# Kernel optimization log

Measured on AMD Instinct MI355X. Metric: run time of the kernel, lower is better.

## Reference

```python
import jax, jax.numpy as jnp
import numpy as np

B, N, DEG = 64, 512, 16        # graphs, nodes per graph, avg degree
C, HID = 10, 128               # input feat dim (== num_classes quirk), hidden
E = B * N * DEG                # total edges (fixed; pooling masks edges)


def _gcn(x, W, b, src, dst, emask, n):
    # PyG GCNConv: add self-loops, symmetric norm D^-1/2 (A+I) D^-1/2 (XW) + b
    h = x @ W
    deg = jax.ops.segment_sum(emask, dst, num_segments=n) + 1.0  # +1 self-loop
    dinv = jax.lax.rsqrt(deg)
    norm = dinv[src] * dinv[dst] * emask
    agg = jax.ops.segment_sum(h[src] * norm[:, None], dst, num_segments=n)
    return agg + h * (dinv * dinv)[:, None] + b  # self-loop term + bias


def _sag_pool(x, src, dst, emask, Wp, bp, n_per):
    # SAGPooling: score = tanh(GCN(x)); per-graph top-k (ratio=0.5); x' = x[perm]*score
    n = x.shape[0]
    score = jnp.tanh(_gcn(x, Wp, bp, src, dst, emask, n)[:, 0])
    k = n_per // 2
    vals, idx = jax.lax.top_k(score.reshape(B, n_per), k)  # [B,k]
    perm = (idx + (jnp.arange(B) * n_per)[:, None]).reshape(-1)
    xk = x[perm] * vals.reshape(-1)[:, None]
    # relabel edges; drop edges touching removed nodes via mask (fixed E)
    mapping = jnp.full((n,), -1, jnp.int32).at[perm].set(
        jnp.arange(B * k, dtype=jnp.int32))
    ns, nd = mapping[src], mapping[dst]
    nmask = emask * ((ns >= 0) & (nd >= 0)).astype(emask.dtype)
    return xk, jnp.maximum(ns, 0), jnp.maximum(nd, 0), nmask, k


def _readout(x, k):
    # global max pool || global mean pool (all kept nodes are real, no padding)
    xg = x.reshape(B, k, -1)
    return jnp.concatenate([xg.max(axis=1), xg.mean(axis=1)], axis=1)


def setup_inputs() -> dict:
    key = jax.random.key(0)
    ks = jax.random.split(key, 16)
    x = jax.random.normal(ks[0], (B * N, C), jnp.float32)
    off = jnp.repeat(jnp.arange(B, dtype=jnp.int32) * N, N * DEG)
    src = jax.random.randint(ks[1], (E,), 0, N, jnp.int32) + off
    dst = jax.random.randint(ks[2], (E,), 0, N, jnp.int32) + off
    p = lambda k, s: jax.random.normal(k, s, jnp.float32) * 0.05
    return {
        "x": x, "src": src, "dst": dst,
        "W1": p(ks[3], (C, HID)), "b1": jnp.zeros((HID,), jnp.float32),
        "W2": p(ks[4], (HID, HID)), "b2": jnp.zeros((HID,), jnp.float32),
        "W3": p(ks[5], (HID, HID)), "b3": jnp.zeros((HID,), jnp.float32),
        "Wp": p(ks[6], (HID, 1)), "bp": jnp.zeros((1,), jnp.float32),
        "L1W": p(ks[7], (2 * HID, HID)), "L1b": jnp.zeros((HID,), jnp.float32),
        "L2W": p(ks[8], (HID, HID // 2)), "L2b": jnp.zeros((HID // 2,), jnp.float32),
    }


def reference(x, src, dst, W1, b1, W2, b2, W3, b3, Wp, bp, L1W, L1b, L2W, L2b):
    emask = jnp.ones((E,), jnp.float32)
    h = jax.nn.relu(_gcn(x, W1, b1, src, dst, emask, B * N))
    h, src, dst, emask, k = _sag_pool(h, src, dst, emask, Wp, bp, N)
    x1 = _readout(h, k)
    h = jax.nn.relu(_gcn(h, W2, b2, src, dst, emask, B * k))
    h, src, dst, emask, k = _sag_pool(h, src, dst, emask, Wp, bp, k)
    x2 = _readout(h, k)
    h = jax.nn.relu(_gcn(h, W3, b3, src, dst, emask, B * k))
    h, src, dst, emask, k = _sag_pool(h, src, dst, emask, Wp, bp, k)
    x3 = _readout(h, k)
    z = x1 + x2 + x3
    z = jax.nn.relu(z @ L1W + L1b)
    # dropout inactive in eval mode
    z = jax.nn.relu(z @ L2W + L2b)
    return jax.nn.log_softmax(z, axis=1)
```

## Files before the change

### kernel.cpp

```cpp
#include <hip/hip_runtime.h>
#include <math.h>

#define BGR 64
#define N0 512
#define E_TOT (BGR*N0*16)
#define EPG 8192
#define EIT 16
#define HID 128


__global__ __launch_bounds__(512) void k_topo0(
    const int* __restrict__ s0, const int* __restrict__ d0,
    int2* __restrict__ edges, int* __restrict__ cnt, int* __restrict__ rowptr,
    float* __restrict__ dinv, int2* __restrict__ csr, float* __restrict__ z){
  __shared__ int   deg[512];
  __shared__ int   sb[512];
  __shared__ int   cur[512];
  __shared__ float dl[512];
  int g = (blockIdx.x & 7)*8 + (blockIdx.x >> 3);
  int t = threadIdx.x;
  int gbase = g*N0, ebase = g*EPG;
  deg[t] = 0;
  if (t < 256) z[g*256 + t] = 0.f;
  __syncthreads();
  int2 ebuf[EIT];
  #pragma unroll
  for (int it = 0; it < EIT; it++){
    int i = ebase + it*512 + t;
    int2 e = make_int2(s0[i], d0[i]);
    ebuf[it] = e;
    edges[i] = e;
    atomicAdd(&deg[e.y - gbase], 1);
  }
  __syncthreads();
  int vdeg = deg[t];
  sb[t] = vdeg; __syncthreads();
  for (int off = 1; off < 512; off <<= 1){
    int add = (t >= off) ? sb[t-off] : 0;
    __syncthreads(); sb[t] += add; __syncthreads();
  }
  int excl = sb[t] - vdeg;
  rowptr[gbase + t] = ebase + excl;
  cnt[gbase + t] = vdeg;
  cur[t] = excl;
  float dv = rsqrtf((float)vdeg + 1.f);
  dl[t] = dv;
  dinv[gbase + t] = dv;
  __syncthreads();
  #pragma unroll
  for (int it = 0; it < EIT; it++){
    int2 e = ebuf[it];
    int sl = e.x - gbase, dc = e.y - gbase;
    int pos = atomicAdd(&cur[dc], 1);
    csr[ebase + pos] = make_int2(e.x, __float_as_int(dl[sl]*dl[dc]));
  }
}

__global__ __launch_bounds__(512) void k_l1_fused(
    const float* __restrict__ x, const float* __restrict__ W1,
    const int2* __restrict__ csr, const int* __restrict__ rowptr,
    const int* __restrict__ cnt, const float* __restrict__ dinv,
    const float* __restrict__ b1, const float* __restrict__ Wp,
    float4* __restrict__ gout4, float* __restrict__ hp_part){
  extern __shared__ float hl[];
  int b = blockIdx.x;
  int xcd = b & 7, idx = b >> 3;
  int graph = xcd*8 + (idx >> 2);
  int qf = idx & 3;
  int t = threadIdx.x;
  int gbase = graph*N0;
  int fp = t & 31;
  int f = qf*32 + fp;
  float wcol[10];
  #pragma unroll
  for (int k = 0; k < 10; k++) wcol[k] = W1[k*HID + f];
  for (int n = t >> 5; n < N0; n += 16){
    const float* xr = x + (gbase + n)*10;
    float acc = 0.f;
    #pragma unroll
    for (int k = 0; k < 10; k++) acc += xr[k]*wcol[k];
    hl[n*32 + fp] = acc;
  }
  __syncthreads();
  const float4* hl4 = (const float4*)hl;
  int l = t & 7, grp = t >> 3;
  float4 bb = ((const float4*)b1)[qf*8 + l];
  float4 wp = ((const float4*)Wp)[qf*8 + l];
  for (int nl = grp; nl < N0; nl += 64){
    int node = gbase + nl;
    int start = rowptr[node], c = cnt[node];
    float4 acc = make_float4(0.f,0.f,0.f,0.f);
    for (int j = 0; j < c; j++){
      int2 e = csr[start + j];
      float wgt = __int_as_float(e.y);
      float4 hv = hl4[(e.x - gbase)*8 + l];
      acc.x += wgt*hv.x; acc.y += wgt*hv.y; acc.z += wgt*hv.z; acc.w += wgt*hv.w;
    }
    float di = dinv[node], dd = di*di;
    float4 hs = hl4[nl*8 + l];
    float4 v;
    v.x = fmaxf(acc.x + hs.x*dd + bb.x, 0.f);
    v.y = fmaxf(acc.y + hs.y*dd + bb.y, 0.f);
    v.z = fmaxf(acc.z + hs.z*dd + bb.z, 0.f);
    v.w = fmaxf(acc.w + hs.w*dd + bb.w, 0.f);
    gout4[node*32 + qf*8 + l] = v;
    float contrib = v.x*wp.x + v.y*wp.y + v.z*wp.z + v.w*wp.w;
    #pragma unroll
    for (int off = 4; off; off >>= 1) contrib += __shfl_down(contrib, off, 8);
    if (l == 0) hp_part[qf*32768 + node] = contrib;
  }
}

__global__ __launch_bounds__(512) void k_lx_fused(
    const float* __restrict__ x, const float* __restrict__ W,
    const int2* __restrict__ csr, const int* __restrict__ rowptr,
    const int* __restrict__ cnt, const float* __restrict__ dinv,
    const float* __restrict__ bia, const float* __restrict__ Wp,
    float4* __restrict__ gout4, float* __restrict__ hp_part, int nper){
  extern __shared__ float smem[];
  float* wl = smem;
  float* hl = smem + 4096;
  int b = blockIdx.x;
  int xcd = b & 7, idx = b >> 3;
  int graph = xcd*8 + (idx >> 2);
  int qf = idx & 3;
  int t = threadIdx.x;
  int gbase = graph*nper;
  int fp = t & 31, f = qf*32 + fp, gi = t >> 5;
  for (int kk = gi; kk < 128; kk += 16) wl[kk*32 + fp] = W[kk*HID + f];
  __syncthreads();
  int npg = nper >> 4;
  for (int n0 = gi*npg; n0 < (gi+1)*npg; n0 += 8){
    float acc[8] = {0,0,0,0,0,0,0,0};
    const float4* xr0 = (const float4*)(x + (gbase + n0)*HID);
    for (int kk = 0; kk < 32; kk++){
      float4 xv[8];
      #pragma unroll
      for (int nd = 0; nd < 8; nd++) xv[nd] = xr0[nd*32 + kk];
      float w0 = wl[(kk*4+0)*32 + fp];
      float w1 = wl[(kk*4+1)*32 + fp];
      float w2 = wl[(kk*4+2)*32 + fp];
      float w3 = wl[(kk*4+3)*32 + fp];
      #pragma unroll
      for (int nd = 0; nd < 8; nd++)
        acc[nd] += xv[nd].x*w0 + xv[nd].y*w1 + xv[nd].z*w2 + xv[nd].w*w3;
    }
    #pragma unroll
    for (int nd = 0; nd < 8; nd++) hl[(n0+nd)*32 + fp] = acc[nd];
  }
  __syncthreads();
  const float4* hl4 = (const float4*)hl;
  int l = t & 7, grp = t >> 3;
  float4 bb = ((const float4*)bia)[qf*8 + l];
  float4 wp = ((const float4*)Wp)[qf*8 + l];
  for (int nl = grp; nl < nper; nl += 64){
    int node = gbase + nl;
    int start = rowptr[node], c = cnt[node];
    float4 acc = make_float4(0.f,0.f,0.f,0.f);
    for (int j = 0; j < c; j++){
      int2 e = csr[start + j];
      float wgt = __int_as_float(e.y);
      float4 hv = hl4[(e.x - gbase)*8 + l];
      acc.x += wgt*hv.x; acc.y += wgt*hv.y; acc.z += wgt*hv.z; acc.w += wgt*hv.w;
    }
    float di = dinv[node], dd = di*di;
    float4 hs = hl4[nl*8 + l];
    float4 v;
    v.x = fmaxf(acc.x + hs.x*dd + bb.x, 0.f);
    v.y = fmaxf(acc.y + hs.y*dd + bb.y, 0.f);
    v.z = fmaxf(acc.z + hs.z*dd + bb.z, 0.f);
    v.w = fmaxf(acc.w + hs.w*dd + bb.w, 0.f);
    gout4[node*32 + qf*8 + l] = v;
    float contrib = v.x*wp.x + v.y*wp.y + v.z*wp.z + v.w*wp.w;
    #pragma unroll
    for (int off = 4; off; off >>= 1) contrib += __shfl_down(contrib, off, 8);
    if (l == 0) hp_part[qf*32768 + node] = contrib;
  }
}

__global__ __launch_bounds__(512) void k_mega(
    const float4* __restrict__ gout4, const float* __restrict__ hp_part,
    int2* __restrict__ csr, int* __restrict__ rowptr, int* __restrict__ cnt,
    float* __restrict__ dinv, const float* __restrict__ bp,
    int2* __restrict__ edges, float4* __restrict__ xpool4,
    float* __restrict__ z, int nper, int lastlev,
    const float* __restrict__ L1W, const float* __restrict__ L1b,
    const float* __restrict__ L2W, const float* __restrict__ L2b,
    float* __restrict__ out){
  __shared__ float sv[512];
  __shared__ int   si[512];
  __shared__ float hpl[512];
  __shared__ int   map[512];
  __shared__ int   sb[512];
  __shared__ int   cur[256];
  __shared__ float dl[256];
  __shared__ float4 pmx[16][32];
  __shared__ float4 psm[16][32];
  __shared__ float zr[256];
  __shared__ float h1[128];
  __shared__ float h2[64];
  __shared__ float red[2];
  int g = (blockIdx.x & 7)*8 + (blockIdx.x >> 3);
  int t = threadIdx.x;
  int k = nper >> 1;
  int gbase = g*nper, ebase = g*EPG, gb2 = g*k;
  bool act = t < nper;
  if (act){
    int node = gbase + t;
    hpl[t] = hp_part[node] + hp_part[32768 + node]
           + hp_part[65536 + node] + hp_part[98304 + node];
  }
  __syncthreads();
  float v = 0.f; int idx = t;
  if (act){
    int start = rowptr[gbase + t], c = cnt[gbase + t];
    float a = 0.f;
    for (int j = 0; j < c; j++){
      int2 e = csr[start + j];
      a += __int_as_float(e.y) * hpl[e.x - gbase];
    }
    float di = dinv[gbase + t];
    v = tanhf(a + hpl[t]*di*di + bp[0]);
  }
  for (int kk = 2; kk <= nper; kk <<= 1){
    for (int jj = kk >> 1; jj > 0; jj >>= 1){
      if (jj >= 64){
        if (act){ sv[t] = v; si[t] = idx; }
        __syncthreads();
        if (act){
          int p = t ^ jj;
          float pv = sv[p]; int pi = si[p];
          bool amLower = (t & jj) == 0;
          bool dirDesc = (t & kk) == 0;
          bool betterMine = (v > pv) || (v == pv && idx < pi);
          if ((amLower == dirDesc) != betterMine){ v = pv; idx = pi; }
        }
        __syncthreads();
      } else if (act){
        float pv = __shfl_xor(v, jj);
        int   pi = __shfl_xor(idx, jj);
        bool amLower = (t & jj) == 0;
        bool dirDesc = (t & kk) == 0;
        bool betterMine = (v > pv) || (v == pv && idx < pi);
        if ((amLower == dirDesc) != betterMine){ v = pv; idx = pi; }
      }
    }
  }
  if (act){ sv[t] = v; si[t] = idx; }
  __syncthreads();
  int l = t & 31, j0 = t >> 5;
  float4 mx = make_float4(-INFINITY,-INFINITY,-INFINITY,-INFINITY);
  float4 sm = make_float4(0.f,0.f,0.f,0.f);
  for (int j = j0; j < k; j += 16){
    float val = sv[j]; int row = si[j];
    float4 hv = gout4[(gbase + row)*32 + l];
    float4 o = make_float4(hv.x*val, hv.y*val, hv.z*val, hv.w*val);
    if (!lastlev) xpool4[(gb2 + j)*32 + l] = o;
    mx.x = fmaxf(mx.x, o.x); mx.y = fmaxf(mx.y, o.y);
    mx.z = fmaxf(mx.z, o.z); mx.w = fmaxf(mx.w, o.w);
    sm.x += o.x; sm.y += o.y; sm.z += o.z; sm.w += o.w;
  }
  pmx[j0][l] = mx; psm[j0][l] = sm;
  __syncthreads();
  if (t < 32){
    float4 M = pmx[0][t], S = psm[0][t];
    #pragma unroll
    for (int q = 1; q < 16; q++){
      float4 m2 = pmx[q][t], s2 = psm[q][t];
      M.x = fmaxf(M.x, m2.x); M.y = fmaxf(M.y, m2.y);
      M.z = fmaxf(M.z, m2.z); M.w = fmaxf(M.w, m2.w);
      S.x += s2.x; S.y += s2.y; S.z += s2.z; S.w += s2.w;
    }
    float ki = 1.f/(float)k;
    float* zp = z + g*256;
    if (!lastlev){
      zp[t*4+0] += M.x; zp[t*4+1] += M.y; zp[t*4+2] += M.z; zp[t*4+3] += M.w;
      zp[128+t*4+0] += S.x*ki; zp[128+t*4+1] += S.y*ki;
      zp[128+t*4+2] += S.z*ki; zp[128+t*4+3] += S.w*ki;
    } else {
      zr[t*4+0] = zp[t*4+0] + M.x; zr[t*4+1] = zp[t*4+1] + M.y;
      zr[t*4+2] = zp[t*4+2] + M.z; zr[t*4+3] = zp[t*4+3] + M.w;
      zr[128+t*4+0] = zp[128+t*4+0] + S.x*ki;
      zr[128+t*4+1] = zp[128+t*4+1] + S.y*ki;
      zr[128+t*4+2] = zp[128+t*4+2] + S.z*ki;
      zr[128+t*4+3] = zp[128+t*4+3] + S.w*ki;
    }
  }
  if (lastlev){
    __syncthreads();
    if (t < 128){
      float a = L1b[t];
      for (int i = 0; i < 256; i++) a += zr[i]*L1W[i*128 + t];
      h1[t] = fmaxf(a, 0.f);
    }
    __syncthreads();
    if (t < 64){
      float a = L2b[t];
      for (int i = 0; i < 128; i++) a += h1[i]*L2W[i*64 + t];
      h2[t] = fmaxf(a, 0.f);
    }
    __syncthreads();
    if (t == 0){
      float mxv = -INFINITY;
      for (int i = 0; i < 64; i++) mxv = fmaxf(mxv, h2[i]);
      float s = 0.f;
      for (int i = 0; i < 64; i++) s += expf(h2[i] - mxv);
      red[0] = mxv; red[1] = logf(s);
    }
    __syncthreads();
    if (t < 64) out[g*64 + t] = h2[t] - red[0] - red[1];
    return;
  }
  if (act) map[t] = -1;
  if (t < k) sb[t] = 0;
  __syncthreads();
  if (t < k) map[si[t]] = t;
  __syncthreads();
  int2 ebuf[EIT];
  #pragma unroll
  for (int it = 0; it < EIT; it++){
    int i = ebase + it*512 + t;
    int2 e = edges[i];
    int2 ne = make_int2(-1, 0);
    if (e.x >= 0){
      int ns = map[e.x - gbase], nd = map[e.y - gbase];
      if (ns >= 0 && nd >= 0){
        ne = make_int2(gb2 + ns, gb2 + nd);
        atomicAdd(&sb[nd], 1);
      }
    }
    ebuf[it] = ne;
    edges[i] = ne;
  }
  __syncthreads();
  int vdeg = (t < k) ? sb[t] : 0;
  for (int off = 1; off < k; off <<= 1){
    int add = (t >= off && t < k) ? sb[t-off] : 0;
    __syncthreads();
    if (t < k) sb[t] += add;
    __syncthreads();
  }
  if (t < k){
    int excl = sb[t] - vdeg;
    rowptr[gb2 + t] = ebase + excl;
    cnt[gb2 + t] = vdeg;
    cur[t] = excl;
    float dv = rsqrtf((float)vdeg + 1.f);
    dl[t] = dv;
    dinv[gb2 + t] = dv;
  }
  __syncthreads();
  #pragma unroll
  for (int it = 0; it < EIT; it++){
    int2 e = ebuf[it];
    if (e.x >= 0){
      int sl = e.x - gb2, dc = e.y - gb2;
      int pos = atomicAdd(&cur[dc], 1);
      csr[ebase + pos] = make_int2(e.x, __float_as_int(dl[sl]*dl[dc]));
    }
  }
}

extern "C" void kernel_launch(void* const* d_in, const int* in_sizes, int n_in,
                              void* d_out, int out_size, void* d_ws, size_t ws_size,
                              hipStream_t stream){
  (void)in_sizes; (void)n_in; (void)out_size; (void)ws_size;
  const float* x0  = (const float*)d_in[0];
  const int*   s0  = (const int*)  d_in[1];
  const int*   d0  = (const int*)  d_in[2];
  const float* W1  = (const float*)d_in[3];  const float* b1 = (const float*)d_in[4];
  const float* W2  = (const float*)d_in[5];  const float* b2 = (const float*)d_in[6];
  const float* W3  = (const float*)d_in[7];  const float* b3 = (const float*)d_in[8];
  const float* Wp  = (const float*)d_in[9];  const float* bp = (const float*)d_in[10];
  const float* L1W = (const float*)d_in[11]; const float* L1b = (const float*)d_in[12];
  const float* L2W = (const float*)d_in[13]; const float* L2b = (const float*)d_in[14];
  float* out = (float*)d_out;

  float* w = (float*)d_ws;
  float* gout  = w; w += 32768*HID;
  float* xpA   = w; w += 16384*HID;
  float* xpB   = w; w += 8192*HID;
  float* dinvv = w; w += 32768;
  float* hppt  = w; w += 4*32768;
  float* z     = w; w += BGR*256;
  int* cnt     = (int*)w; w += 32768;
  int* rowptr  = (int*)w; w += 32768;
  int2* edges  = (int2*)w; w += 2*E_TOT;
  int2* csr    = (int2*)w; w += 2*E_TOT;

  k_topo0<<<BGR, 512, 0, stream>>>(s0, d0, edges, cnt, rowptr, dinvv, csr, z);

  k_l1_fused<<<256, 512, 65536, stream>>>(x0, W1, csr, rowptr, cnt, dinvv,
                                          b1, Wp, (float4*)gout, hppt);
  k_mega<<<BGR, 512, 0, stream>>>((const float4*)gout, hppt, csr, rowptr, cnt,
                                  dinvv, bp, edges, (float4*)xpA, z, 512, 0,
                                  L1W, L1b, L2W, L2b, out);
  k_lx_fused<<<256, 512, (4096 + 256*32)*4, stream>>>(xpA, W2, csr, rowptr, cnt,
                                                      dinvv, b2, Wp, (float4*)gout,
                                                      hppt, 256);
  k_mega<<<BGR, 512, 0, stream>>>((const float4*)gout, hppt, csr, rowptr, cnt,
                                  dinvv, bp, edges, (float4*)xpB, z, 256, 0,
                                  L1W, L1b, L2W, L2b, out);
  k_lx_fused<<<256, 512, (4096 + 128*32)*4, stream>>>(xpB, W3, csr, rowptr, cnt,
                                                      dinvv, b3, Wp, (float4*)gout,
                                                      hppt, 128);
  k_mega<<<BGR, 512, 0, stream>>>((const float4*)gout, hppt, csr, rowptr, cnt,
                                  dinvv, bp, edges, (float4*)xpA, z, 128, 1,
                                  L1W, L1b, L2W, L2b, out);
}
```

Measured before the change: 266.7 us.

## Split feature dimension into 8 slices of 16 and cooperatively load CSR edges

The fused GCN layer kernels now split the 128 hidden features into eight 16-wide slices instead of four 32-wide ones. This doubles the grid to 512 blocks and halves shared memory per block, aiming for more occupancy and parallelism on the 256 CUs. The neighbor gather now loads 8 edges cooperatively across the 8-lane group and broadcasts them with shuffles, removing redundant per-lane CSR loads. The pooling kernel sums 8 partial score buffers and unrolls its edge loop by 4. The cost is twice the CSR traversal and twice the X re-reads across slices, plus more partial-sum traffic.

Measured after the change: 271.0 us. About the same (+1.6%).

```diff
diff --git a/kernel.cpp b/kernel.cpp
--- a/kernel.cpp
+++ b/kernel.cpp
@@ -7,6 +7,7 @@
 #define EPG 8192
 #define EIT 16
 #define HID 128
+#define SW 16
 
 
 __global__ __launch_bounds__(512) void k_topo0(
@@ -56,59 +57,73 @@
   }
 }
 
+__device__ __forceinline__ void gather_slice(
+    const float* hl, const int2* __restrict__ csr,
+    const int* __restrict__ rowptr, const int* __restrict__ cnt,
+    const float* __restrict__ dinv, const float* __restrict__ bia,
+    const float* __restrict__ Wp, float* __restrict__ gout,
+    float* __restrict__ hp_part, int gbase, int nper, int slice,
+    int l, int grp){
+  const float2* hl2 = (const float2*)hl;
+  float2 bb = ((const float2*)bia)[slice*8 + l];
+  float2 wp = ((const float2*)Wp)[slice*8 + l];
+  for (int nl = grp; nl < nper; nl += 64){
+    int node = gbase + nl;
+    int start = rowptr[node], c = cnt[node];
+    float ax = 0.f, ay = 0.f;
+    for (int jb = 0; jb < c; jb += 8){
+      int2 e = make_int2(0, 0);
+      if (jb + l < c) e = csr[start + jb + l];
+      int nb = c - jb; if (nb > 8) nb = 8;
+      for (int j = 0; j < nb; j++){
+        int   sx  = __shfl(e.x, j, 8);
+        float wgt = __int_as_float(__shfl(e.y, j, 8));
+        float2 hv = hl2[(sx - gbase)*8 + l];
+        ax += wgt*hv.x; ay += wgt*hv.y;
+      }
+    }
+    float di = dinv[node], dd = di*di;
+    float2 hs = hl2[nl*8 + l];
+    float2 v;
+    v.x = fmaxf(ax + hs.x*dd + bb.x, 0.f);
+    v.y = fmaxf(ay + hs.y*dd + bb.y, 0.f);
+    ((float2*)gout)[node*64 + slice*8 + l] = v;
+    float contrib = v.x*wp.x + v.y*wp.y;
+    contrib += __shfl_down(contrib, 4, 8);
+    contrib += __shfl_down(contrib, 2, 8);
+    contrib += __shfl_down(contrib, 1, 8);
+    if (l == 0) hp_part[slice*32768 + node] = contrib;
+  }
+}
+
 __global__ __launch_bounds__(512) void k_l1_fused(
     const float* __restrict__ x, const float* __restrict__ W1,
     const int2* __restrict__ csr, const int* __restrict__ rowptr,
     const int* __restrict__ cnt, const float* __restrict__ dinv,
     const float* __restrict__ b1, const float* __restrict__ Wp,
-    float4* __restrict__ gout4, float* __restrict__ hp_part){
+    float* __restrict__ gout, float* __restrict__ hp_part){
   extern __shared__ float hl[];
   int b = blockIdx.x;
   int xcd = b & 7, idx = b >> 3;
-  int graph = xcd*8 + (idx >> 2);
-  int qf = idx & 3;
+  int graph = xcd*8 + (idx >> 3);
+  int slice = idx & 7;
   int t = threadIdx.x;
   int gbase = graph*N0;
-  int fp = t & 31;
-  int f = qf*32 + fp;
+  int fp = t & 15, gi = t >> 4;
+  int f = slice*SW + fp;
   float wcol[10];
   #pragma unroll
   for (int k = 0; k < 10; k++) wcol[k] = W1[k*HID + f];
-  for (int n = t >> 5; n < N0; n += 16){
+  for (int n = gi*16; n < gi*16 + 16; n++){
     const float* xr = x + (gbase + n)*10;
     float acc = 0.f;
     #pragma unroll
     for (int k = 0; k < 10; k++) acc += xr[k]*wcol[k];
-    hl[n*32 + fp] = acc;
-  }
-  __syncthreads();
-  const float4* hl4 = (const float4*)hl;
-  int l = t & 7, grp = t >> 3;
-  float4 bb = ((const float4*)b1)[qf*8 + l];
-  float4 wp = ((const float4*)Wp)[qf*8 + l];
-  for (int nl = grp; nl < N0; nl += 64){
-    int node = gbase + nl;
-    int start = rowptr[node], c = cnt[node];
-    float4 acc = make_float4(0.f,0.f,0.f,0.f);
-    for (int j = 0; j < c; j++){
-      int2 e = csr[start + j];
-      float wgt = __int_as_float(e.y);
-      float4 hv = hl4[(e.x - gbase)*8 + l];
-      acc.x += wgt*hv.x; acc.y += wgt*hv.y; acc.z += wgt*hv.z; acc.w += wgt*hv.w;
-    }
-    float di = dinv[node], dd = di*di;
-    float4 hs = hl4[nl*8 + l];
-    float4 v;
-    v.x = fmaxf(acc.x + hs.x*dd + bb.x, 0.f);
-    v.y = fmaxf(acc.y + hs.y*dd + bb.y, 0.f);
-    v.z = fmaxf(acc.z + hs.z*dd + bb.z, 0.f);
-    v.w = fmaxf(acc.w + hs.w*dd + bb.w, 0.f);
-    gout4[node*32 + qf*8 + l] = v;
-    float contrib = v.x*wp.x + v.y*wp.y + v.z*wp.z + v.w*wp.w;
-    #pragma unroll
-    for (int off = 4; off; off >>= 1) contrib += __shfl_down(contrib, off, 8);
-    if (l == 0) hp_part[qf*32768 + node] = contrib;
-  }
+    hl[n*SW + fp] = acc;
+  }
+  __syncthreads();
+  gather_slice(hl, csr, rowptr, cnt, dinv, b1, Wp, gout, hp_part,
+               gbase, N0, slice, t & 7, t >> 3);
 }
 
 __global__ __launch_bounds__(512) void k_lx_fused(
@@ -116,66 +131,41 @@
     const int2* __restrict__ csr, const int* __restrict__ rowptr,
     const int* __restrict__ cnt, const float* __restrict__ dinv,
     const float* __restrict__ bia, const float* __restrict__ Wp,
-    float4* __restrict__ gout4, float* __restrict__ hp_part, int nper){
+    float* __restrict__ gout, float* __restrict__ hp_part, int nper){
   extern __shared__ float smem[];
   float* wl = smem;
-  float* hl = smem + 4096;
+  float* hl = smem + 2048;
   int b = blockIdx.x;
   int xcd = b & 7, idx = b >> 3;
-  int graph = xcd*8 + (idx >> 2);
-  int qf = idx & 3;
+  int graph = xcd*8 + (idx >> 3);
+  int slice = idx & 7;
   int t = threadIdx.x;
   int gbase = graph*nper;
-  int fp = t & 31, f = qf*32 + fp, gi = t >> 5;
-  for (int kk = gi; kk < 128; kk += 16) wl[kk*32 + fp] = W[kk*HID + f];
-  __syncthreads();
-  int npg = nper >> 4;
-  for (int n0 = gi*npg; n0 < (gi+1)*npg; n0 += 8){
-    float acc[8] = {0,0,0,0,0,0,0,0};
+  int fp = t & 15, gi = t >> 4, f = slice*SW + fp;
+  for (int kk = gi; kk < 128; kk += 32) wl[kk*SW + fp] = W[kk*HID + f];
+  __syncthreads();
+  int npg = nper >> 5;
+  for (int n0 = gi*npg; n0 < (gi+1)*npg; n0 += 4){
+    float acc[4] = {0,0,0,0};
     const float4* xr0 = (const float4*)(x + (gbase + n0)*HID);
     for (int kk = 0; kk < 32; kk++){
-      float4 xv[8];
+      float4 xv[4];
       #pragma unroll
-      for (int nd = 0; nd < 8; nd++) xv[nd] = xr0[nd*32 + kk];
-      float w0 = wl[(kk*4+0)*32 + fp];
-      float w1 = wl[(kk*4+1)*32 + fp];
-      float w2 = wl[(kk*4+2)*32 + fp];
-      float w3 = wl[(kk*4+3)*32 + fp];
+      for (int nd = 0; nd < 4; nd++) xv[nd] = xr0[nd*32 + kk];
+      float w0 = wl[(kk*4+0)*SW + fp];
+      float w1 = wl[(kk*4+1)*SW + fp];
+      float w2 = wl[(kk*4+2)*SW + fp];
+      float w3 = wl[(kk*4+3)*SW + fp];
       #pragma unroll
-      for (int nd = 0; nd < 8; nd++)
+      for (int nd = 0; nd < 4; nd++)
         acc[nd] += xv[nd].x*w0 + xv[nd].y*w1 + xv[nd].z*w2 + xv[nd].w*w3;
     }
     #pragma unroll
-    for (int nd = 0; nd < 8; nd++) hl[(n0+nd)*32 + fp] = acc[nd];
-  }
-  __syncthreads();
-  const float4* hl4 = (const float4*)hl;
-  int l = t & 7, grp = t >> 3;
-  float4 bb = ((const float4*)bia)[qf*8 + l];
-  float4 wp = ((const float4*)Wp)[qf*8 + l];
-  for (int nl = grp; nl < nper; nl += 64){
-    int node = gbase + nl;
-    int start = rowptr[node], c = cnt[node];
-    float4 acc = make_float4(0.f,0.f,0.f,0.f);
-    for (int j = 0; j < c; j++){
-      int2 e = csr[start + j];
-      float wgt = __int_as_float(e.y);
-      float4 hv = hl4[(e.x - gbase)*8 + l];
-      acc.x += wgt*hv.x; acc.y += wgt*hv.y; acc.z += wgt*hv.z; acc.w += wgt*hv.w;
-    }
-    float di = dinv[node], dd = di*di;
-    float4 hs = hl4[nl*8 + l];
-    float4 v;
-    v.x = fmaxf(acc.x + hs.x*dd + bb.x, 0.f);
-    v.y = fmaxf(acc.y + hs.y*dd + bb.y, 0.f);
-    v.z = fmaxf(acc.z + hs.z*dd + bb.z, 0.f);
-    v.w = fmaxf(acc.w + hs.w*dd + bb.w, 0.f);
-    gout4[node*32 + qf*8 + l] = v;
-    float contrib = v.x*wp.x + v.y*wp.y + v.z*wp.z + v.w*wp.w;
-    #pragma unroll
-    for (int off = 4; off; off >>= 1) contrib += __shfl_down(contrib, off, 8);
-    if (l == 0) hp_part[qf*32768 + node] = contrib;
-  }
+    for (int nd = 0; nd < 4; nd++) hl[(n0+nd)*SW + fp] = acc[nd];
+  }
+  __syncthreads();
+  gather_slice(hl, csr, rowptr, cnt, dinv, bia, Wp, gout, hp_part,
+               gbase, nper, slice, t & 7, t >> 3);
 }
 
 __global__ __launch_bounds__(512) void k_mega(
@@ -207,17 +197,28 @@
   bool act = t < nper;
   if (act){
     int node = gbase + t;
-    hpl[t] = hp_part[node] + hp_part[32768 + node]
-           + hp_part[65536 + node] + hp_part[98304 + node];
+    float s = 0.f;
+    #pragma unroll
+    for (int q = 0; q < 8; q++) s += hp_part[q*32768 + node];
+    hpl[t] = s;
   }
   __syncthreads();
   float v = 0.f; int idx = t;
   if (act){
     int start = rowptr[gbase + t], c = cnt[gbase + t];
     float a = 0.f;
-    for (int j = 0; j < c; j++){
+    int j = 0;
+    for (; j + 4 <= c; j += 4){
+      int2 e0 = csr[start+j],   e1 = csr[start+j+1];
+      int2 e2 = csr[start+j+2], e3 = csr[start+j+3];
+      a += __int_as_float(e0.y)*hpl[e0.x - gbase]
+         + __int_as_float(e1.y)*hpl[e1.x - gbase]
+         + __int_as_float(e2.y)*hpl[e2.x - gbase]
+         + __int_as_float(e3.y)*hpl[e3.x - gbase];
+    }
+    for (; j < c; j++){
       int2 e = csr[start + j];
-      a += __int_as_float(e.y) * hpl[e.x - gbase];
+      a += __int_as_float(e.y)*hpl[e.x - gbase];
     }
     float di = dinv[gbase + t];
     v = tanhf(a + hpl[t]*di*di + bp[0]);
@@ -381,7 +382,7 @@
   float* xpA   = w; w += 16384*HID;
   float* xpB   = w; w += 8192*HID;
   float* dinvv = w; w += 32768;
-  float* hppt  = w; w += 4*32768;
+  float* hppt  = w; w += 8*32768;
   float* z     = w; w += BGR*256;
   int* cnt     = (int*)w; w += 32768;
   int* rowptr  = (int*)w; w += 32768;
@@ -390,19 +391,19 @@
 
   k_topo0<<<BGR, 512, 0, stream>>>(s0, d0, edges, cnt, rowptr, dinvv, csr, z);
 
-  k_l1_fused<<<256, 512, 65536, stream>>>(x0, W1, csr, rowptr, cnt, dinvv,
-                                          b1, Wp, (float4*)gout, hppt);
+  k_l1_fused<<<512, 512, N0*SW*4, stream>>>(x0, W1, csr, rowptr, cnt, dinvv,
+                                            b1, Wp, gout, hppt);
   k_mega<<<BGR, 512, 0, stream>>>((const float4*)gout, hppt, csr, rowptr, cnt,
                                   dinvv, bp, edges, (float4*)xpA, z, 512, 0,
                                   L1W, L1b, L2W, L2b, out);
-  k_lx_fused<<<256, 512, (4096 + 256*32)*4, stream>>>(xpA, W2, csr, rowptr, cnt,
-                                                      dinvv, b2, Wp, (float4*)gout,
+  k_lx_fused<<<512, 512, (2048 + 256*SW)*4, stream>>>(xpA, W2, csr, rowptr, cnt,
+                                                      dinvv, b2, Wp, gout,
                                                       hppt, 256);
   k_mega<<<BGR, 512, 0, stream>>>((const float4*)gout, hppt, csr, rowptr, cnt,
                                   dinvv, bp, edges, (float4*)xpB, z, 256, 0,
                                   L1W, L1b, L2W, L2b, out);
-  k_lx_fused<<<256, 512, (4096 + 128*32)*4, stream>>>(xpB, W3, csr, rowptr, cnt,
-                                                      dinvv, b3, Wp, (float4*)gout,
+  k_lx_fused<<<512, 512, (2048 + 128*SW)*4, stream>>>(xpB, W3, csr, rowptr, cnt,
+                                                      dinvv, b3, Wp, gout,
                                                       hppt, 128);
   k_mega<<<BGR, 512, 0, stream>>>((const float4*)gout, hppt, csr, rowptr, cnt,
                                   dinvv, bp, edges, (float4*)xpA, z, 128, 1,
```
